# Optimization experiments

Measured on AMD Instinct MI355X. Metric: run time of the kernel, lower is better.

## Reference

```python
import jax, jax.numpy as jnp
import numpy as np

N_HEAD = 16
N_EMBD = 2048
HEAD_DIM = N_EMBD // N_HEAD


def setup_inputs() -> dict:
    key = jax.random.key(0)
    kx, kqkv, kp = jax.random.split(key, 3)
    B, S = 2, 2048
    x = jax.random.normal(kx, (B, S, N_EMBD), dtype=jnp.float32)
    # torch nn.Linear weights, stored as [out, in]; y = x @ W.T
    scale = 1.0 / np.sqrt(N_EMBD)
    Wqkv = jax.random.uniform(kqkv, (3 * N_EMBD, N_EMBD), dtype=jnp.float32, minval=-scale, maxval=scale)
    Wproj = jax.random.uniform(kp, (N_EMBD, N_EMBD), dtype=jnp.float32, minval=-scale, maxval=scale)
    return {"x": x, "Wqkv": Wqkv, "Wproj": Wproj}


def reference(x, Wqkv, Wproj):
    B, S, E = x.shape
    qkv = x @ Wqkv.T  # [B,S,3E]
    q, k, v = jnp.split(qkv, 3, axis=2)
    # [B,H,S,D]
    q = q.reshape(B, S, N_HEAD, HEAD_DIM).transpose(0, 2, 1, 3)
    k = k.reshape(B, S, N_HEAD, HEAD_DIM).transpose(0, 2, 1, 3)
    v = v.reshape(B, S, N_HEAD, HEAD_DIM).transpose(0, 2, 1, 3)
    scores = jnp.einsum('bhqd,bhkd->bhqk', q, k) / jnp.sqrt(jnp.float32(HEAD_DIM))
    causal = jnp.tril(jnp.ones((S, S), dtype=bool))  # [S,S]
    scores = jnp.where(causal[None, None, :, :], scores, -jnp.inf)
    weights = jax.nn.softmax(scores, axis=-1)
    out = jnp.einsum('bhqk,bhkd->bhqd', weights, v)  # [B,H,S,D]
    out = out.transpose(0, 2, 1, 3).reshape(B, S, E)
    return out @ Wproj.T
```

## Files before the change

### kernel.cpp

```cpp
#include <hip/hip_runtime.h>
#include <cstdint>
#include <cstddef>

typedef __bf16 bf16;
typedef __bf16 bf16x8 __attribute__((ext_vector_type(8)));
typedef float  f32x4  __attribute__((ext_vector_type(4)));

static_assert(sizeof(bf16x8) == 16, "bf16x8 must be 16B");

__device__ __forceinline__ void async_copy16(const bf16* g, bf16* l) {
  __builtin_amdgcn_global_load_lds(
      (__attribute__((address_space(1))) void*)(g),
      (__attribute__((address_space(3))) void*)(l),
      16, 0, 0);
}

__global__ __launch_bounds__(256)
void conv_f32_bf16(const float* __restrict__ s, bf16* __restrict__ d) {
  const size_t i = ((size_t)blockIdx.x * 256 + threadIdx.x) * 8;
  const f32x4 a = *(const f32x4*)(s + i);
  const f32x4 b = *(const f32x4*)(s + i + 4);
  bf16x8 o;
#pragma unroll
  for (int e = 0; e < 4; ++e) { o[e] = (bf16)a[e]; o[4 + e] = (bf16)b[e]; }
  *(bf16x8*)(d + i) = o;
}

template<int AMODE, int CMODE>
__global__ __launch_bounds__(256, 2)
void gemm_bt(const bf16* __restrict__ A, const bf16* __restrict__ W,
             float* __restrict__ Crow, bf16* __restrict__ Cq,
             bf16* __restrict__ Ck, bf16* __restrict__ Cvt,
             int M, int N, int K, int nbase) {
  __shared__ bf16 As[128 * 64];
  __shared__ bf16 Ws[128 * 64];

  const int tid  = threadIdx.x;
  const int wave = tid >> 6;
  const int lane = tid & 63;
  const int quad = lane >> 4;
  const int r    = lane & 15;
  const int m0 = blockIdx.y * 128;
  const int n0 = blockIdx.x * 128;
  const int wm = (wave >> 1) * 64;
  const int wn = (wave & 1) * 64;

  const int lrow   = lane >> 3;
  const int gchunk = (lane & 7) ^ lrow;

  f32x4 acc[4][4] = {};

  for (int k0 = 0; k0 < K; k0 += 64) {
    __syncthreads();
    for (int j = 0; j < 4; ++j) {
      const int rbase = (wave * 4 + j) * 8;
      const int rowA  = m0 + rbase + lrow;
      const bf16* aSrc;
      if constexpr (AMODE == 2) {
        const int b = rowA >> 11, s = rowA & 2047;
        aSrc = A + ((size_t)(b * 16 + (k0 >> 7)) * 2048 + s) * 128
                 + (k0 & 127) + gchunk * 8;
      } else {
        aSrc = A + (size_t)rowA * K + k0 + gchunk * 8;
      }
      async_copy16(aSrc, As + rbase * 64);
      async_copy16(W + (size_t)(n0 + rbase + lrow) * K + k0 + gchunk * 8,
                   Ws + rbase * 64);
    }
    __syncthreads();
    for (int ks = 0; ks < 2; ++ks) {
      bf16x8 af[4], bfv[4];
      for (int i = 0; i < 4; ++i) {
        const int ar = wm + i * 16 + r;
        af[i]  = *(const bf16x8*)(As + ar * 64 + (((ks * 4 + quad) ^ (ar & 7)) * 8));
        const int br = wn + i * 16 + r;
        bfv[i] = *(const bf16x8*)(Ws + br * 64 + (((ks * 4 + quad) ^ (br & 7)) * 8));
      }
      for (int i = 0; i < 4; ++i)
        for (int j = 0; j < 4; ++j)
          acc[i][j] = __builtin_amdgcn_mfma_f32_16x16x32_bf16(af[i], bfv[j], acc[i][j], 0, 0, 0);
    }
  }

  for (int i = 0; i < 4; ++i) {
    const int growb = m0 + wm + i * 16 + quad * 4;
    for (int j = 0; j < 4; ++j) {
      const int gcol = n0 + wn + j * 16 + r;
      for (int rg = 0; rg < 4; ++rg) {
        const int grow = growb + rg;
        if constexpr (CMODE == 1) {
          const int gc = nbase + gcol;
          const int which = gc >> 11;
          const int h = (gc >> 7) & 15;
          const int d = gc & 127;
          const int b = grow >> 11;
          const int s = grow & 2047;
          const bf16 v = (bf16)acc[i][j][rg];
          if (which == 0)
            Cq[(((size_t)b * 16 + h) * 2048 + s) * 128 + d] = v;
          else if (which == 1)
            Ck[(((size_t)b * 16 + h) * 2048 + s) * 128 + d] = v;
          else
            Cvt[(((size_t)b * 16 + h) * 128 + d) * 2048 + s] = v;
        } else {
          Crow[(size_t)grow * N + gcol] = acc[i][j][rg];
        }
      }
    }
  }
}

__global__ __launch_bounds__(512, 2)
void attn_kernel(bf16* __restrict__ Q, const bf16* __restrict__ K,
                 const bf16* __restrict__ Vt, int S) {
  __shared__ bf16 k_lds[2][64 * 128];
  __shared__ bf16 v_lds[2][128 * 64];
  __shared__ bf16 p_lds[8][16 * 64];

  const int tid = threadIdx.x, wave = tid >> 6, lane = tid & 63;
  const int quad = lane >> 4, r = lane & 15;
  const int bh = blockIdx.y;
  bf16* Qh = Q + (size_t)bh * S * 128;
  const bf16* Kh = K + (size_t)bh * S * 128;
  const bf16* Vth = Vt + (size_t)bh * 128 * S;

  const float sc = 0.0883883476483184f * 1.4426950408889634f;

  auto issue_stage = [&](int kv0, int buf) {
#pragma unroll
    for (int j = 0; j < 2; ++j) {
      const int lin0 = j * 512 + wave * 64;
      const int lin = lin0 + lane;
      const int row = lin >> 4, ch = lin & 15;
      async_copy16(Kh + (size_t)(kv0 + row) * 128 + ((ch ^ (row & 7)) << 3),
                   &k_lds[buf][0] + lin0 * 8);
    }
#pragma unroll
    for (int j = 0; j < 2; ++j) {
      const int lin0 = j * 512 + wave * 64;
      const int lin = lin0 + lane;
      const int row = lin >> 3, c = lin & 7;
      async_copy16(Vth + (size_t)row * S + kv0 + ((c ^ (row & 7)) << 3),
                   &v_lds[buf][0] + lin0 * 8);
    }
  };

  for (int pass = 0; pass < 2; ++pass) {
    const int qb = pass ? blockIdx.x : (15 - blockIdx.x);
    const int q0 = qb << 7;
    const int qrow0 = q0 + wave * 16;
    const int nkv = (q0 + 128) >> 6;

    bf16x8 qf[4];
    for (int ks = 0; ks < 4; ++ks)
      qf[ks] = *(const bf16x8*)(Qh + (size_t)(qrow0 + r) * 128 + ks * 32 + quad * 8);

    f32x4 o_acc[8] = {};
    f32x4 m_run, l_run;
    for (int t = 0; t < 4; ++t) { m_run[t] = -1e30f; l_run[t] = 0.f; }

    issue_stage(0, 0);

    for (int kt = 0; kt < nkv; ++kt) {
      const int kv0 = kt << 6;
      const int cur = kt & 1;
      if (kt + 1 < nkv) {
        issue_stage((kt + 1) << 6, cur ^ 1);
        asm volatile("s_waitcnt vmcnt(4)" ::: "memory");
      } else {
        asm volatile("s_waitcnt vmcnt(0)" ::: "memory");
      }
      __builtin_amdgcn_sched_barrier(0);
      __syncthreads();

      if (kv0 <= qrow0 + 15) {
        f32x4 sa[4] = {};
        __builtin_amdgcn_s_setprio(1);
        for (int ks = 0; ks < 4; ++ks) {
          bf16x8 kf[4];
          for (int nt = 0; nt < 4; ++nt) {
            const int kr = nt * 16 + r;
            kf[nt] = *(const bf16x8*)(&k_lds[cur][0] + kr * 128 + (((ks * 4 + quad) ^ (kr & 7)) << 3));
          }
          for (int nt = 0; nt < 4; ++nt)
            sa[nt] = __builtin_amdgcn_mfma_f32_16x16x32_bf16(qf[ks], kf[nt], sa[nt], 0, 0, 0);
        }
        __builtin_amdgcn_s_setprio(0);
        if (kv0 + 63 > qrow0) {
          for (int nt = 0; nt < 4; ++nt) {
            const int col  = kv0 + nt * 16 + r;
            const int rowb = qrow0 + quad * 4;
            for (int rg = 0; rg < 4; ++rg)
              if (col > rowb + rg) sa[nt][rg] = -1e30f;
          }
        }
        f32x4 mx = sa[0];
        for (int nt = 1; nt < 4; ++nt)
          for (int rg = 0; rg < 4; ++rg) mx[rg] = fmaxf(mx[rg], sa[nt][rg]);
        for (int off = 1; off < 16; off <<= 1)
          for (int rg = 0; rg < 4; ++rg) mx[rg] = fmaxf(mx[rg], __shfl_xor(mx[rg], off, 64));
        float need = mx[0] - m_run[0];
        for (int rg = 1; rg < 4; ++rg) need = fmaxf(need, mx[rg] - m_run[rg]);
        if (need * sc > 8.0f) {
          f32x4 alpha;
          for (int rg = 0; rg < 4; ++rg) {
            const float mnew = fmaxf(m_run[rg], mx[rg]);
            alpha[rg] = exp2f((m_run[rg] - mnew) * sc);
            m_run[rg] = mnew;
            l_run[rg] *= alpha[rg];
          }
          for (int nt2 = 0; nt2 < 8; ++nt2)
            for (int rg = 0; rg < 4; ++rg) o_acc[nt2][rg] *= alpha[rg];
        }
        f32x4 rsum = {0.f, 0.f, 0.f, 0.f};
        for (int nt = 0; nt < 4; ++nt)
          for (int rg = 0; rg < 4; ++rg) {
            const float p = exp2f((sa[nt][rg] - m_run[rg]) * sc);
            sa[nt][rg] = p;
            rsum[rg] += p;
          }
        for (int off = 1; off < 16; off <<= 1)
          for (int rg = 0; rg < 4; ++rg) rsum[rg] += __shfl_xor(rsum[rg], off, 64);
        for (int rg = 0; rg < 4; ++rg) l_run[rg] += rsum[rg];
        for (int nt = 0; nt < 4; ++nt)
          for (int rg = 0; rg < 4; ++rg) {
            const int prow = quad * 4 + rg;
            const int pcol = nt * 16 + r;
            p_lds[wave][prow * 64 + (((pcol >> 3) ^ (prow & 7)) * 8) + (pcol & 7)] =
                (bf16)sa[nt][rg];
          }
        __builtin_amdgcn_s_setprio(1);
        for (int ks2 = 0; ks2 < 2; ++ks2) {
          const int prow = r;
          const bf16x8 pf = *(const bf16x8*)(p_lds[wave] + prow * 64 + (((ks2 * 4 + quad) ^ (prow & 7)) * 8));
          for (int nt2 = 0; nt2 < 8; ++nt2) {
            const int vrow = nt2 * 16 + r;
            const bf16x8 vf = *(const bf16x8*)(&v_lds[cur][0] + vrow * 64 + (((ks2 * 4 + quad) ^ (vrow & 7)) * 8));
            o_acc[nt2] = __builtin_amdgcn_mfma_f32_16x16x32_bf16(pf, vf, o_acc[nt2], 0, 0, 0);
          }
        }
        __builtin_amdgcn_s_setprio(0);
      }
      __syncthreads();
    }

    f32x4 inv;
    for (int rg = 0; rg < 4; ++rg) inv[rg] = 1.0f / l_run[rg];
    for (int nt2 = 0; nt2 < 8; ++nt2) {
      const int d = nt2 * 16 + r;
      for (int rg = 0; rg < 4; ++rg) {
        const int s = qrow0 + quad * 4 + rg;
        Qh[(size_t)s * 128 + d] = (bf16)(o_acc[nt2][rg] * inv[rg]);
      }
    }
  }
}

extern "C" void kernel_launch(void* const* d_in, const int* in_sizes, int n_in,
                              void* d_out, int out_size, void* d_ws, size_t ws_size,
                              hipStream_t stream) {
  const float* x     = (const float*)d_in[0];
  const float* Wqkv  = (const float*)d_in[1];
  const float* Wproj = (const float*)d_in[2];
  float* out = (float*)d_out;

  const int Bm = 4096, E = 2048;
  const size_t plane = 8388608;

  bf16* qw  = (bf16*)d_ws;
  bf16* vtw = qw + plane;
  bf16* xb  = vtw + plane;
  bf16* kw  = (bf16*)d_out;
  bf16* wqb = kw + plane;

  conv_f32_bf16<<<8388608 / 2048, 256, 0, stream>>>(x, xb);
  conv_f32_bf16<<<6291456 / 2048, 256, 0, stream>>>(Wqkv, wqb);
  gemm_bt<0, 1><<<dim3(3072 / 128, Bm / 128), 256, 0, stream>>>(
      xb, wqb, nullptr, qw, kw, vtw, Bm, 3072, E, 0);
  conv_f32_bf16<<<6291456 / 2048, 256, 0, stream>>>(Wqkv + 6291456, wqb);
  gemm_bt<0, 1><<<dim3(3072 / 128, Bm / 128), 256, 0, stream>>>(
      xb, wqb, nullptr, qw, kw, vtw, Bm, 3072, E, 3072);
  attn_kernel<<<dim3(8, 32), 512, 0, stream>>>(qw, kw, vtw, 2048);
  conv_f32_bf16<<<4194304 / 2048, 256, 0, stream>>>(Wproj, xb);
  gemm_bt<2, 0><<<dim3(2048 / 128, Bm / 128), 256, 0, stream>>>(
      qw, xb, out, nullptr, nullptr, nullptr, Bm, 2048, E, 0);
}
```

Measured before the change: 412.5 us.

## Replace GEMM with 256x256-tile double-buffered pipelined kernel and XCD-aware block remap

Replaces the 128x128 single-buffered GEMM with a 512-thread, 256x256-tile kernel. It double-buffers K tiles in LDS and issues async global-to-LDS loads split into phases interleaved with MFMA work, using explicit vmcnt waits, barriers and setprio. It also remaps workgroup IDs in strides of 8, apparently to spread work across chiplets. The aim is to hide global memory latency and raise data reuse per block, at the cost of 128KB of LDS and fewer blocks, which lowers occupancy and wave-level parallelism on the smaller grids.

```diff
diff --git a/kernel.cpp b/kernel.cpp
--- a/kernel.cpp
+++ b/kernel.cpp
@@ -26,66 +26,130 @@
   *(bf16x8*)(d + i) = o;
 }
 
+template<int AMODE>
+__device__ __forceinline__ void stage_half(const bf16* __restrict__ P, int K,
+                                           int row0, int k0, int ks,
+                                           bf16* lds, int wave, int lane) {
+#pragma unroll
+  for (int i = 0; i < 2; ++i) {
+    const int lin0 = i * 512 + wave * 64;
+    const int lin  = lin0 + lane;
+    const int row  = lin >> 2;
+    const int ch   = lin & 3;
+    const int gch  = ch ^ ((row >> 1) & 3);
+    const bf16* src;
+    if constexpr (AMODE == 2) {
+      const int rowA = row0 + row;
+      const int b = rowA >> 11, s = rowA & 2047;
+      const int kk = k0 + ks * 32;
+      src = P + ((size_t)(b * 16 + (kk >> 7)) * 2048 + s) * 128 + (kk & 127) + gch * 8;
+    } else {
+      src = P + (size_t)(row0 + row) * K + k0 + ks * 32 + gch * 8;
+    }
+    async_copy16(src, lds + ks * 8192 + lin0 * 8);
+  }
+}
+
 template<int AMODE, int CMODE>
-__global__ __launch_bounds__(256, 2)
-void gemm_bt(const bf16* __restrict__ A, const bf16* __restrict__ W,
+__global__ __launch_bounds__(512, 2)
+void gemm256(const bf16* __restrict__ A, const bf16* __restrict__ W,
              float* __restrict__ Crow, bf16* __restrict__ Cq,
              bf16* __restrict__ Ck, bf16* __restrict__ Cvt,
              int M, int N, int K, int nbase) {
-  __shared__ bf16 As[128 * 64];
-  __shared__ bf16 Ws[128 * 64];
+  __shared__ bf16 As[2 * 16384];
+  __shared__ bf16 Ws[2 * 16384];
 
   const int tid  = threadIdx.x;
-  const int wave = tid >> 6;
-  const int lane = tid & 63;
-  const int quad = lane >> 4;
-  const int r    = lane & 15;
-  const int m0 = blockIdx.y * 128;
-  const int n0 = blockIdx.x * 128;
-  const int wm = (wave >> 1) * 64;
-  const int wn = (wave & 1) * 64;
-
-  const int lrow   = lane >> 3;
-  const int gchunk = (lane & 7) ^ lrow;
-
-  f32x4 acc[4][4] = {};
-
-  for (int k0 = 0; k0 < K; k0 += 64) {
-    __syncthreads();
-    for (int j = 0; j < 4; ++j) {
-      const int rbase = (wave * 4 + j) * 8;
-      const int rowA  = m0 + rbase + lrow;
-      const bf16* aSrc;
-      if constexpr (AMODE == 2) {
-        const int b = rowA >> 11, s = rowA & 2047;
-        aSrc = A + ((size_t)(b * 16 + (k0 >> 7)) * 2048 + s) * 128
-                 + (k0 & 127) + gchunk * 8;
+  const int wave = tid >> 6, lane = tid & 63;
+  const int quad = lane >> 4, r = lane & 15;
+  const int wr = wave >> 2, wc = wave & 3;
+
+  const int gx  = gridDim.x;
+  const int nwg = gx * gridDim.y;
+  int wg = blockIdx.y * gx + blockIdx.x;
+  wg = (wg & 7) * (nwg >> 3) + (wg >> 3);
+  const int m0 = (wg / gx) * 256;
+  const int n0 = (wg % gx) * 256;
+
+  const int wm = wr * 128;
+  const int wn = wc * 64;
+  const int nT = K >> 6;
+
+  f32x4 acc[8][4] = {};
+
+  stage_half<AMODE>(A, K, m0, 0, 0, As, wave, lane);
+  stage_half<0>   (W, K, n0, 0, 0, Ws, wave, lane);
+  stage_half<AMODE>(A, K, m0, 0, 1, As, wave, lane);
+  stage_half<0>   (W, K, n0, 0, 1, Ws, wave, lane);
+  if (nT > 1) {
+    stage_half<AMODE>(A, K, m0, 64, 0, As + 16384, wave, lane);
+    stage_half<0>   (W, K, n0, 64, 0, Ws + 16384, wave, lane);
+    asm volatile("s_waitcnt vmcnt(4)" ::: "memory");
+  } else {
+    asm volatile("s_waitcnt vmcnt(0)" ::: "memory");
+  }
+  __builtin_amdgcn_s_barrier();
+
+  for (int t = 0; t < nT; ++t) {
+    const int c = t & 1;
+    bf16* Ab = As + c * 16384;
+    bf16* Wb = Ws + c * 16384;
+    bf16* An = As + (c ^ 1) * 16384;
+    bf16* Wn = Ws + (c ^ 1) * 16384;
+    bf16x8 af[4], bfr[4];
+#pragma unroll
+    for (int ph = 0; ph < 4; ++ph) {
+      const int ks = ph >> 1, mh = ph & 1;
+      if (mh == 0) {
+#pragma unroll
+        for (int n = 0; n < 4; ++n) {
+          const int br = wn + n * 16 + r;
+          bfr[n] = *(const bf16x8*)(Wb + ks * 8192 + br * 32 + ((quad ^ ((br >> 1) & 3)) << 3));
+        }
+      }
+#pragma unroll
+      for (int m = 0; m < 4; ++m) {
+        const int ar = wm + mh * 64 + m * 16 + r;
+        af[m] = *(const bf16x8*)(Ab + ks * 8192 + ar * 32 + ((quad ^ ((ar >> 1) & 3)) << 3));
+      }
+      if (ph == 0) {
+        if (t + 1 < nT) stage_half<AMODE>(A, K, m0, (t + 1) << 6, 1, An, wave, lane);
+      } else if (ph == 1) {
+        if (t + 1 < nT) stage_half<0>(W, K, n0, (t + 1) << 6, 1, Wn, wave, lane);
+      } else if (ph == 2) {
+        if (t + 2 < nT) stage_half<AMODE>(A, K, m0, (t + 2) << 6, 0, Ab, wave, lane);
       } else {
-        aSrc = A + (size_t)rowA * K + k0 + gchunk * 8;
-      }
-      async_copy16(aSrc, As + rbase * 64);
-      async_copy16(W + (size_t)(n0 + rbase + lrow) * K + k0 + gchunk * 8,
-                   Ws + rbase * 64);
-    }
-    __syncthreads();
-    for (int ks = 0; ks < 2; ++ks) {
-      bf16x8 af[4], bfv[4];
-      for (int i = 0; i < 4; ++i) {
-        const int ar = wm + i * 16 + r;
-        af[i]  = *(const bf16x8*)(As + ar * 64 + (((ks * 4 + quad) ^ (ar & 7)) * 8));
-        const int br = wn + i * 16 + r;
-        bfv[i] = *(const bf16x8*)(Ws + br * 64 + (((ks * 4 + quad) ^ (br & 7)) * 8));
-      }
-      for (int i = 0; i < 4; ++i)
-        for (int j = 0; j < 4; ++j)
-          acc[i][j] = __builtin_amdgcn_mfma_f32_16x16x32_bf16(af[i], bfv[j], acc[i][j], 0, 0, 0);
-    }
-  }
-
-  for (int i = 0; i < 4; ++i) {
+        if (t + 2 < nT) {
+          stage_half<0>(W, K, n0, (t + 2) << 6, 0, Wb, wave, lane);
+          __builtin_amdgcn_sched_barrier(0);
+          asm volatile("s_waitcnt vmcnt(4)" ::: "memory");
+        } else if (t + 1 < nT) {
+          __builtin_amdgcn_sched_barrier(0);
+          asm volatile("s_waitcnt vmcnt(0)" ::: "memory");
+        }
+      }
+      __builtin_amdgcn_s_barrier();
+      asm volatile("s_waitcnt lgkmcnt(0)" ::: "memory");
+      __builtin_amdgcn_sched_barrier(0);
+      __builtin_amdgcn_s_setprio(1);
+#pragma unroll
+      for (int m = 0; m < 4; ++m)
+#pragma unroll
+        for (int n = 0; n < 4; ++n)
+          acc[mh * 4 + m][n] =
+              __builtin_amdgcn_mfma_f32_16x16x32_bf16(af[m], bfr[n], acc[mh * 4 + m][n], 0, 0, 0);
+      __builtin_amdgcn_s_setprio(0);
+      __builtin_amdgcn_s_barrier();
+    }
+  }
+
+#pragma unroll
+  for (int i = 0; i < 8; ++i) {
     const int growb = m0 + wm + i * 16 + quad * 4;
+#pragma unroll
     for (int j = 0; j < 4; ++j) {
       const int gcol = n0 + wn + j * 16 + r;
+#pragma unroll
       for (int rg = 0; rg < 4; ++rg) {
         const int grow = growb + rg;
         if constexpr (CMODE == 1) {
@@ -275,13 +339,13 @@
 
   conv_f32_bf16<<<8388608 / 2048, 256, 0, stream>>>(x, xb);
   conv_f32_bf16<<<6291456 / 2048, 256, 0, stream>>>(Wqkv, wqb);
-  gemm_bt<0, 1><<<dim3(3072 / 128, Bm / 128), 256, 0, stream>>>(
+  gemm256<0, 1><<<dim3(3072 / 256, Bm / 256), 512, 0, stream>>>(
       xb, wqb, nullptr, qw, kw, vtw, Bm, 3072, E, 0);
   conv_f32_bf16<<<6291456 / 2048, 256, 0, stream>>>(Wqkv + 6291456, wqb);
-  gemm_bt<0, 1><<<dim3(3072 / 128, Bm / 128), 256, 0, stream>>>(
+  gemm256<0, 1><<<dim3(3072 / 256, Bm / 256), 512, 0, stream>>>(
       xb, wqb, nullptr, qw, kw, vtw, Bm, 3072, E, 3072);
   attn_kernel<<<dim3(8, 32), 512, 0, stream>>>(qw, kw, vtw, 2048);
   conv_f32_bf16<<<4194304 / 2048, 256, 0, stream>>>(Wproj, xb);
-  gemm_bt<2, 0><<<dim3(2048 / 128, Bm / 128), 256, 0, stream>>>(
+  gemm256<2, 0><<<dim3(2048 / 256, Bm / 256), 512, 0, stream>>>(
       qw, xb, out, nullptr, nullptr, nullptr, Bm, 2048, E, 0);
 }
```

After: 450.2 us. 9.1% more time.
